# Kernel optimization log

Hardware: AMD Instinct MI355X
Metric: run time of the kernel (lower is better)

Reference implementation:

```python
import jax, jax.numpy as jnp
from jax import lax
import numpy as np

B, L, F = 4, 1024, 32
DM, NL, DS, DC, EX, NH = 256, 4, 16, 4, 2, 4
DI = EX * DM            # 512 inner channels
DTR = (DM + 15) // 16   # dt_rank = 16


def setup_inputs() -> dict:
    key = jax.random.key(0)
    ks = jax.random.split(key, 12)
    s = 0.02
    rn = lambda k, shape: jax.random.normal(k, shape, jnp.float32) * s
    return dict(
        x=jax.random.normal(ks[0], (B, L, F), jnp.float32),
        proj_w=rn(ks[1], (DM, F)), proj_b=jnp.zeros((DM,), jnp.float32),
        inproj_w=rn(ks[2], (NL, 2 * DI, DM)),
        conv_w=rn(ks[3], (NL, DI, DC)), conv_b=jnp.zeros((NL, DI), jnp.float32),
        xproj_w=rn(ks[4], (NL, DTR + 2 * DS, DI)),
        dtproj_w=rn(ks[5], (NL, DI, DTR)), dtproj_b=rn(ks[6], (NL, DI)),
        A_log=jnp.tile(jnp.log(jnp.arange(1, DS + 1, dtype=jnp.float32))[None, None, :], (NL, DI, 1)),
        Dp=jnp.ones((NL, DI), jnp.float32),
        outproj_w=rn(ks[7], (NL, DM, DI)),
        ln_g=jnp.ones((NL, DM), jnp.float32), ln_b=jnp.zeros((NL, DM), jnp.float32),
        head_w1=rn(ks[8], (DM, DM)), head_b1=jnp.zeros((DM,), jnp.float32),
        head_w2=rn(ks[9], (NH, DM)), head_b2=jnp.zeros((NH,), jnp.float32),
    )


def _layernorm(x, g, b, eps=1e-5):
    mu = x.mean(axis=-1, keepdims=True)
    var = ((x - mu) ** 2).mean(axis=-1, keepdims=True)
    return (x - mu) * lax.rsqrt(var + eps) * g + b


def _mamba(x, inw, cw, cb, xpw, dtw, dtb, A_log, Dp, outw):
    b, l, _ = x.shape
    xz = x @ inw.T                       # (b,l,2*DI)
    u, z = xz[..., :DI], xz[..., DI:]
    # causal depthwise conv1d, kernel DC
    up = jnp.pad(u, ((0, 0), (DC - 1, 0), (0, 0)))
    uc = sum(up[:, k:k + l, :] * cw[:, k] for k in range(DC)) + cb
    uc = jax.nn.silu(uc)
    dbc = uc @ xpw.T                     # (b,l,DTR+2*DS)
    dt, Bc, Cc = dbc[..., :DTR], dbc[..., DTR:DTR + DS], dbc[..., DTR + DS:]
    delta = jax.nn.softplus(dt @ dtw.T + dtb)   # (b,l,DI)
    A = -jnp.exp(A_log)                  # (DI,DS)

    def step(h, inp):
        d_t, B_t, C_t, u_t = inp         # (b,DI),(b,DS),(b,DS),(b,DI)
        h = jnp.exp(d_t[..., None] * A) * h + (d_t * u_t)[..., None] * B_t[:, None, :]
        return h, jnp.einsum('bdn,bn->bd', h, C_t)

    h0 = jnp.zeros((b, DI, DS), x.dtype)
    xs = tuple(jnp.swapaxes(a, 0, 1) for a in (delta, Bc, Cc, uc))
    _, ys = lax.scan(step, h0, xs)       # ys: (l,b,DI)
    y = jnp.swapaxes(ys, 0, 1) + uc * Dp
    return (y * jax.nn.silu(z)) @ outw.T


def reference(x, proj_w, proj_b, inproj_w, conv_w, conv_b, xproj_w, dtproj_w, dtproj_b,
              A_log, Dp, outproj_w, ln_g, ln_b, head_w1, head_b1, head_w2, head_b2):
    h = x @ proj_w.T + proj_b
    for i in range(NL):
        blk = _mamba(h, inproj_w[i], conv_w[i], conv_b[i], xproj_w[i],
                     dtproj_w[i], dtproj_b[i], A_log[i], Dp[i], outproj_w[i])
        h = h + _layernorm(blk, ln_g[i], ln_b[i])
    p = h.mean(axis=1)                   # (b,DM) pool over time
    hid = jax.nn.relu(p @ head_w1.T + head_b1)
    return hid @ head_w2.T + head_b2     # (b,NH)
```

## Files before the change

kernel.cpp:

```cpp
#include <hip/hip_runtime.h>
#include <hip/hip_fp16.h>
#include <math.h>

#define LTOT 1024
#define BB   4
#define F_IN 32
#define DM   256
#define DI   512
#define DS   16
#define DTRN 16
#define NXP  48
#define NLAY 4
#define NH   4
#define NC   16
#define CLEN 64
#define ROWS (BB*LTOT)

typedef _Float16 half8 __attribute__((ext_vector_type(8)));
typedef float f32x16 __attribute__((ext_vector_type(16)));
typedef unsigned short us8 __attribute__((ext_vector_type(8)));

__device__ __forceinline__ float siluf_(float x) { return x / (1.0f + expf(-x)); }
__device__ __forceinline__ float softplusf_(float x) {
    if (x > 20.f) return x;
    if (x < -20.f) return expf(x);
    return log1pf(expf(x));
}

__device__ __forceinline__ void split16(float x, unsigned short& hi, unsigned short& lo) {
    __half h = __float2half(x);
    hi = *(unsigned short*)&h;
    float r = x - __half2float(h);
    __half l = __float2half(r);
    lo = *(unsigned short*)&l;
}

__global__ __launch_bounds__(256) void k_init(const float* __restrict__ x,
                                              const float* __restrict__ pw,
                                              const float* __restrict__ pb,
                                              const float* __restrict__ inw,
                                              const float* __restrict__ outw,
                                              float* __restrict__ h,
                                              unsigned short* __restrict__ hh,
                                              unsigned short* __restrict__ hl,
                                              unsigned short* __restrict__ iwh,
                                              unsigned short* __restrict__ iwl,
                                              unsigned short* __restrict__ owh,
                                              unsigned short* __restrict__ owl) {
    __shared__ float wl[DM][33];
    __shared__ float xl[16][32];
    int bid = blockIdx.x, t = threadIdx.x;
    if (bid < 1536) {
        int q = bid * 256 + t;
        ushort4 h4, l4;
        if (q < 262144) {
            float4 v = ((const float4*)inw)[q];
            split16(v.x, h4.x, l4.x); split16(v.y, h4.y, l4.y);
            split16(v.z, h4.z, l4.z); split16(v.w, h4.w, l4.w);
            *(ushort4*)(iwh + (size_t)q * 4) = h4;
            *(ushort4*)(iwl + (size_t)q * 4) = l4;
        } else {
            int r = q - 262144;
            float4 v = ((const float4*)outw)[r];
            split16(v.x, h4.x, l4.x); split16(v.y, h4.y, l4.y);
            split16(v.z, h4.z, l4.z); split16(v.w, h4.w, l4.w);
            *(ushort4*)(owh + (size_t)r * 4) = h4;
            *(ushort4*)(owl + (size_t)r * 4) = l4;
        }
        return;
    }
    int r0 = (bid - 1536) * 16;
    for (int i = t; i < DM * 32 / 4; i += 256) {
        float4 v = ((const float4*)pw)[i];
        int c = i / 8, k = (i % 8) * 4;
        wl[c][k] = v.x; wl[c][k + 1] = v.y; wl[c][k + 2] = v.z; wl[c][k + 3] = v.w;
    }
    for (int i = t; i < 16 * 32 / 4; i += 256) {
        float4 v = ((const float4*)(x + (size_t)r0 * F_IN))[i];
        int r = i / 8, k = (i % 8) * 4;
        xl[r][k] = v.x; xl[r][k + 1] = v.y; xl[r][k + 2] = v.z; xl[r][k + 3] = v.w;
    }
    __syncthreads();
    int c = t;
    float bias = pb[c];
    float acc[16];
#pragma unroll
    for (int r = 0; r < 16; ++r) acc[r] = bias;
    for (int k = 0; k < 32; ++k) {
        float w = wl[c][k];
#pragma unroll
        for (int r = 0; r < 16; ++r) acc[r] = fmaf(xl[r][k], w, acc[r]);
    }
#pragma unroll
    for (int r = 0; r < 16; ++r) {
        size_t idx = (size_t)(r0 + r) * DM + c;
        h[idx] = acc[r];
        unsigned short vh, vl; split16(acc[r], vh, vl);
        hh[idx] = vh; hl[idx] = vl;
    }
}

__global__ __launch_bounds__(256) void k_gemm_xz(const unsigned short* __restrict__ Ahp,
                                                 const unsigned short* __restrict__ Alp,
                                                 const unsigned short* __restrict__ Bhp,
                                                 const unsigned short* __restrict__ Blp,
                                                 float* __restrict__ C) {
    __shared__ unsigned short Ah[64][40], Al[64][40], Bh[128][40], Bl[128][40];
    int t = threadIdx.x;
    int bx = blockIdx.x & 7;
    int by = blockIdx.x >> 3;
    int rowA = t >> 2, kA = (t & 3) * 8;
    int rowB = t >> 1, kB = (t & 1) * 16;
    const unsigned short* ApH = Ahp + (size_t)(by * 64 + rowA) * DM + kA;
    const unsigned short* ApL = Alp + (size_t)(by * 64 + rowA) * DM + kA;
    const unsigned short* BpH = Bhp + (size_t)(bx * 128 + rowB) * DM + kB;
    const unsigned short* BpL = Blp + (size_t)(bx * 128 + rowB) * DM + kB;
    us8 rah = *(const us8*)ApH, ral = *(const us8*)ApL;
    us8 rbh0 = *(const us8*)BpH, rbh1 = *(const us8*)(BpH + 8);
    us8 rbl0 = *(const us8*)BpL, rbl1 = *(const us8*)(BpL + 8);
    int lane = t & 63, wid = t >> 6;
    int fr = lane & 31, fg = lane >> 5;
    int wr = wid >> 1, wc = wid & 1;
    f32x16 acc[2] = {};
    for (int k0 = 0; k0 < DM; k0 += 32) {
        *(us8*)&Ah[rowA][kA] = rah;
        *(us8*)&Al[rowA][kA] = ral;
        *(us8*)&Bh[rowB][kB] = rbh0; *(us8*)&Bh[rowB][kB + 8] = rbh1;
        *(us8*)&Bl[rowB][kB] = rbl0; *(us8*)&Bl[rowB][kB + 8] = rbl1;
        __syncthreads();
        if (k0 + 32 < DM) {
            rah = *(const us8*)(ApH + k0 + 32); ral = *(const us8*)(ApL + k0 + 32);
            rbh0 = *(const us8*)(BpH + k0 + 32); rbh1 = *(const us8*)(BpH + k0 + 40);
            rbl0 = *(const us8*)(BpL + k0 + 32); rbl1 = *(const us8*)(BpL + k0 + 40);
        }
#pragma unroll
        for (int s = 0; s < 2; ++s) {
            int ko = s * 16 + fg * 8;
            half8 ah = *(const half8*)&Ah[wr * 32 + fr][ko];
            half8 al = *(const half8*)&Al[wr * 32 + fr][ko];
#pragma unroll
            for (int fc = 0; fc < 2; ++fc) {
                half8 bh = *(const half8*)&Bh[wc * 64 + fc * 32 + fr][ko];
                half8 bl = *(const half8*)&Bl[wc * 64 + fc * 32 + fr][ko];
                acc[fc] = __builtin_amdgcn_mfma_f32_32x32x16_f16(ah, bh, acc[fc], 0, 0, 0);
                acc[fc] = __builtin_amdgcn_mfma_f32_32x32x16_f16(ah, bl, acc[fc], 0, 0, 0);
                acc[fc] = __builtin_amdgcn_mfma_f32_32x32x16_f16(al, bh, acc[fc], 0, 0, 0);
            }
        }
        __syncthreads();
    }
    float* Cp = C + (size_t)(by * 64 + wr * 32) * 1024 + bx * 128 + wc * 64;
#pragma unroll
    for (int fc = 0; fc < 2; ++fc) {
#pragma unroll
        for (int reg = 0; reg < 16; ++reg) {
            int row = (reg & 3) + 8 * (reg >> 2) + 4 * fg;
            Cp[(size_t)row * 1024 + fc * 32 + fr] = acc[fc][reg];
        }
    }
}

__global__ __launch_bounds__(256) void k_dbcp(const float* __restrict__ xz,
                                              const float* __restrict__ cw,
                                              const float* __restrict__ cb,
                                              const float* __restrict__ xpw,
                                              float* __restrict__ uc,
                                              float* __restrict__ dbp) {
    __shared__ float us[32][132];
    __shared__ float wsd[48][132];
    int t = threadIdx.x;
    int kp = blockIdx.x & 3;
    int r0 = (blockIdx.x >> 2) * 32;
    int k0 = kp * 128;
    float4* us4 = (float4*)us;
    float4* ws4 = (float4*)wsd;
#pragma unroll
    for (int j = 0; j < 4; ++j) {
        int i = t + j * 256;
        int r = i >> 5, kq = i & 31;
        int rr = r0 + r, d = k0 + kq * 4;
        int tt = rr & (LTOT - 1);
        float4 acc = make_float4(cb[d], cb[d + 1], cb[d + 2], cb[d + 3]);
#pragma unroll
        for (int k = 0; k < 4; ++k) {
            int ts = tt - 3 + k;
            if (ts < 0) continue;
            float4 u = *(const float4*)(xz + (size_t)(rr - 3 + k) * 1024 + d);
            acc.x = fmaf(u.x, cw[(d + 0) * 4 + k], acc.x);
            acc.y = fmaf(u.y, cw[(d + 1) * 4 + k], acc.y);
            acc.z = fmaf(u.z, cw[(d + 2) * 4 + k], acc.z);
            acc.w = fmaf(u.w, cw[(d + 3) * 4 + k], acc.w);
        }
        acc.x = siluf_(acc.x); acc.y = siluf_(acc.y); acc.z = siluf_(acc.z); acc.w = siluf_(acc.w);
        us4[r * 33 + kq] = acc;
        *(float4*)(uc + (size_t)rr * DI + d) = acc;
    }
#pragma unroll
    for (int j = 0; j < 6; ++j) {
        int i = t + j * 256;
        int r = i >> 5, kq = i & 31;
        ws4[r * 33 + kq] = *(const float4*)(xpw + (size_t)r * DI + k0 + kq * 4);
    }
    __syncthreads();
    int tx = t & 15, ty = t >> 4;
    const float4* ua = us4 + (ty * 2) * 33;
    const float4* ub = ua + 33;
    const float4* w0p = ws4 + (tx * 3) * 33;
    const float4* w1p = w0p + 33;
    const float4* w2p = w0p + 66;
    float acc[2][3] = {};
#pragma unroll 4
    for (int kq = 0; kq < 32; ++kq) {
        float4 u0 = ua[kq], u1 = ub[kq];
        float4 w0 = w0p[kq], w1 = w1p[kq], w2 = w2p[kq];
        acc[0][0] = fmaf(u0.x, w0.x, acc[0][0]); acc[0][0] = fmaf(u0.y, w0.y, acc[0][0]);
        acc[0][0] = fmaf(u0.z, w0.z, acc[0][0]); acc[0][0] = fmaf(u0.w, w0.w, acc[0][0]);
        acc[0][1] = fmaf(u0.x, w1.x, acc[0][1]); acc[0][1] = fmaf(u0.y, w1.y, acc[0][1]);
        acc[0][1] = fmaf(u0.z, w1.z, acc[0][1]); acc[0][1] = fmaf(u0.w, w1.w, acc[0][1]);
        acc[0][2] = fmaf(u0.x, w2.x, acc[0][2]); acc[0][2] = fmaf(u0.y, w2.y, acc[0][2]);
        acc[0][2] = fmaf(u0.z, w2.z, acc[0][2]); acc[0][2] = fmaf(u0.w, w2.w, acc[0][2]);
        acc[1][0] = fmaf(u1.x, w0.x, acc[1][0]); acc[1][0] = fmaf(u1.y, w0.y, acc[1][0]);
        acc[1][0] = fmaf(u1.z, w0.z, acc[1][0]); acc[1][0] = fmaf(u1.w, w0.w, acc[1][0]);
        acc[1][1] = fmaf(u1.x, w1.x, acc[1][1]); acc[1][1] = fmaf(u1.y, w1.y, acc[1][1]);
        acc[1][1] = fmaf(u1.z, w1.z, acc[1][1]); acc[1][1] = fmaf(u1.w, w1.w, acc[1][1]);
        acc[1][2] = fmaf(u1.x, w2.x, acc[1][2]); acc[1][2] = fmaf(u1.y, w2.y, acc[1][2]);
        acc[1][2] = fmaf(u1.z, w2.z, acc[1][2]); acc[1][2] = fmaf(u1.w, w2.w, acc[1][2]);
    }
    float* outp = dbp + (size_t)(r0 + ty * 2) * 192 + kp * 48 + tx * 3;
    outp[0] = acc[0][0]; outp[1] = acc[0][1]; outp[2] = acc[0][2];
    outp[192] = acc[1][0]; outp[193] = acc[1][1]; outp[194] = acc[1][2];
}

__global__ __launch_bounds__(256) void k_scanA(const float* __restrict__ dbp,
                                               const float* __restrict__ uc,
                                               const float* __restrict__ dtw,
                                               const float* __restrict__ dtb,
                                               const float* __restrict__ A_log,
                                               float* __restrict__ P,
                                               float* __restrict__ hL) {
    __shared__ float2 du2[CLEN][16];
    __shared__ float  Bl[CLEN][16];
    __shared__ float  dbl[CLEN][17];
    __shared__ float  wdl[16][17];
    __shared__ float  wbias[16];
    int bid = blockIdx.x;
    int c = bid & 15, dblk = (bid >> 4) & 31, b = bid >> 9;
    int d0 = dblk * 16, t0 = c * CLEN;
    int t = threadIdx.x;
    int row = t >> 2, q4 = (t & 3) * 4;
    size_t rbase = (size_t)(b * LTOT + t0 + row);
    float4 uv = *(const float4*)(uc + rbase * DI + d0 + q4);
    {
        const float* pp = dbp + rbase * 192;
        float4 a0 = *(const float4*)(pp + q4);
        float4 a1 = *(const float4*)(pp + 48 + q4);
        float4 a2 = *(const float4*)(pp + 96 + q4);
        float4 a3 = *(const float4*)(pp + 144 + q4);
        dbl[row][q4 + 0] = ((a0.x + a1.x) + a2.x) + a3.x;
        dbl[row][q4 + 1] = ((a0.y + a1.y) + a2.y) + a3.y;
        dbl[row][q4 + 2] = ((a0.z + a1.z) + a2.z) + a3.z;
        dbl[row][q4 + 3] = ((a0.w + a1.w) + a2.w) + a3.w;
        float4 b0 = *(const float4*)(pp + 16 + q4);
        float4 b1 = *(const float4*)(pp + 64 + q4);
        float4 b2 = *(const float4*)(pp + 112 + q4);
        float4 b3 = *(const float4*)(pp + 160 + q4);
        Bl[row][q4 + 0] = ((b0.x + b1.x) + b2.x) + b3.x;
        Bl[row][q4 + 1] = ((b0.y + b1.y) + b2.y) + b3.y;
        Bl[row][q4 + 2] = ((b0.z + b1.z) + b2.z) + b3.z;
        Bl[row][q4 + 3] = ((b0.w + b1.w) + b2.w) + b3.w;
    }
    if (t < 64) {
        int dd = t >> 2, sg = (t & 3) * 4;
        const float* wp = dtw + (size_t)(d0 + dd) * 16 + sg;
        wdl[dd][sg + 0] = wp[0]; wdl[dd][sg + 1] = wp[1];
        wdl[dd][sg + 2] = wp[2]; wdl[dd][sg + 3] = wp[3];
    }
    if (t < 16) wbias[t] = dtb[d0 + t];
    __syncthreads();
    {
        float s0 = wbias[q4 + 0], s1 = wbias[q4 + 1], s2 = wbias[q4 + 2], s3 = wbias[q4 + 3];
#pragma unroll
        for (int k = 0; k < 16; ++k) {
            float dv = dbl[row][k];
            s0 = fmaf(dv, wdl[q4 + 0][k], s0);
            s1 = fmaf(dv, wdl[q4 + 1][k], s1);
            s2 = fmaf(dv, wdl[q4 + 2][k], s2);
            s3 = fmaf(dv, wdl[q4 + 3][k], s3);
        }
        du2[row][q4 + 0] = make_float2(softplusf_(s0), uv.x);
        du2[row][q4 + 1] = make_float2(softplusf_(s1), uv.y);
        du2[row][q4 + 2] = make_float2(softplusf_(s2), uv.z);
        du2[row][q4 + 3] = make_float2(softplusf_(s3), uv.w);
    }
    __syncthreads();
    int n = t & 15, dn = t >> 4;
    float Ac = -expf(A_log[(size_t)(d0 + dn) * DS + n]);
    float h = 0.f, Pp = 1.f;
#pragma unroll 8
    for (int k = 0; k < CLEN; ++k) {
        float2 du = du2[k][dn];
        float Bv = Bl[k][n];
        float a = expf(du.x * Ac);
        Pp *= a;
        h = fmaf(a, h, du.x * du.y * Bv);
    }
    size_t idx = ((size_t)(b * NC + c)) * (DI * DS) + (size_t)d0 * DS + t;
    P[idx] = Pp;
    hL[idx] = h;
}

__global__ __launch_bounds__(256) void k_scanC(const float* __restrict__ dbp,
                                               const float* __restrict__ uc,
                                               const float* __restrict__ dtw,
                                               const float* __restrict__ dtb,
                                               const float* __restrict__ A_log,
                                               const float* __restrict__ P,
                                               const float* __restrict__ hL,
                                               const float* __restrict__ Dp,
                                               const float* __restrict__ xz,
                                               unsigned short* __restrict__ yh,
                                               unsigned short* __restrict__ yl) {
    __shared__ float2 du2[CLEN][16];
    __shared__ float2 bc2[CLEN][16];
    __shared__ float  ytmp[16][16][20];
    float* scr = &ytmp[0][0][0];
    float (*dbl)[17] = (float(*)[17])scr;
    float (*wdl)[17] = (float(*)[17])(scr + 1088);
    float* wbias = scr + 1088 + 272;
    int bid = blockIdx.x;
    int c = bid & 15, dblk = (bid >> 4) & 31, b = bid >> 9;
    int d0 = dblk * 16, t0 = c * CLEN;
    int t = threadIdx.x;
    int row = t >> 2, q4 = (t & 3) * 4;
    size_t rbase = (size_t)(b * LTOT + t0 + row);
    float4 uv = *(const float4*)(uc + rbase * DI + d0 + q4);
    {
        const float* pp = dbp + rbase * 192;
        float4 a0 = *(const float4*)(pp + q4);
        float4 a1 = *(const float4*)(pp + 48 + q4);
        float4 a2 = *(const float4*)(pp + 96 + q4);
        float4 a3 = *(const float4*)(pp + 144 + q4);
        dbl[row][q4 + 0] = ((a0.x + a1.x) + a2.x) + a3.x;
        dbl[row][q4 + 1] = ((a0.y + a1.y) + a2.y) + a3.y;
        dbl[row][q4 + 2] = ((a0.z + a1.z) + a2.z) + a3.z;
        dbl[row][q4 + 3] = ((a0.w + a1.w) + a2.w) + a3.w;
        float4 b0 = *(const float4*)(pp + 16 + q4);
        float4 b1 = *(const float4*)(pp + 64 + q4);
        float4 b2 = *(const float4*)(pp + 112 + q4);
        float4 b3 = *(const float4*)(pp + 160 + q4);
        float4 c0 = *(const float4*)(pp + 32 + q4);
        float4 c1 = *(const float4*)(pp + 80 + q4);
        float4 c2 = *(const float4*)(pp + 128 + q4);
        float4 c3 = *(const float4*)(pp + 176 + q4);
        float B0 = ((b0.x + b1.x) + b2.x) + b3.x, C0 = ((c0.x + c1.x) + c2.x) + c3.x;
        float B1 = ((b0.y + b1.y) + b2.y) + b3.y, C1 = ((c0.y + c1.y) + c2.y) + c3.y;
        float B2 = ((b0.z + b1.z) + b2.z) + b3.z, C2 = ((c0.z + c1.z) + c2.z) + c3.z;
        float B3 = ((b0.w + b1.w) + b2.w) + b3.w, C3 = ((c0.w + c1.w) + c2.w) + c3.w;
        bc2[row][q4 + 0] = make_float2(B0, C0);
        bc2[row][q4 + 1] = make_float2(B1, C1);
        bc2[row][q4 + 2] = make_float2(B2, C2);
        bc2[row][q4 + 3] = make_float2(B3, C3);
    }
    if (t < 64) {
        int dd = t >> 2, sg = (t & 3) * 4;
        const float* wp = dtw + (size_t)(d0 + dd) * 16 + sg;
        wdl[dd][sg + 0] = wp[0]; wdl[dd][sg + 1] = wp[1];
        wdl[dd][sg + 2] = wp[2]; wdl[dd][sg + 3] = wp[3];
    }
    if (t < 16) wbias[t] = dtb[d0 + t];
    __syncthreads();
    {
        float s0 = wbias[q4 + 0], s1 = wbias[q4 + 1], s2 = wbias[q4 + 2], s3 = wbias[q4 + 3];
#pragma unroll
        for (int k = 0; k < 16; ++k) {
            float dv = dbl[row][k];
            s0 = fmaf(dv, wdl[q4 + 0][k], s0);
            s1 = fmaf(dv, wdl[q4 + 1][k], s1);
            s2 = fmaf(dv, wdl[q4 + 2][k], s2);
            s3 = fmaf(dv, wdl[q4 + 3][k], s3);
        }
        du2[row][q4 + 0] = make_float2(softplusf_(s0), uv.x);
        du2[row][q4 + 1] = make_float2(softplusf_(s1), uv.y);
        du2[row][q4 + 2] = make_float2(softplusf_(s2), uv.z);
        du2[row][q4 + 3] = make_float2(softplusf_(s3), uv.w);
    }
    __syncthreads();
    int n = t & 15, dn = t >> 4;
    float Ac = -expf(A_log[(size_t)(d0 + dn) * DS + n]);
    float Hin = 0.f;
    for (int cc = 0; cc < c; ++cc) {
        size_t idx = ((size_t)(b * NC + cc)) * (DI * DS) + (size_t)d0 * DS + t;
        Hin = fmaf(P[idx], Hin, hL[idx]);
    }
    float h = Hin;
    int rdn = t & 15, rk = t >> 4;
    float DpV = Dp[d0 + rdn];
    for (int s = 0; s < CLEN / 16; ++s) {
#pragma unroll
        for (int kk = 0; kk < 16; ++kk) {
            int k = s * 16 + kk;
            float2 du = du2[k][dn];
            float2 bc = bc2[k][n];
            float a = expf(du.x * Ac);
            h = fmaf(a, h, du.x * du.y * bc.x);
            ytmp[kk][dn][n] = h * bc.y;
        }
        __syncthreads();
        {
            const float* rowp = &ytmp[rk][rdn][0];
            float4 v0 = *(const float4*)(rowp + 0);
            float4 v1 = *(const float4*)(rowp + 4);
            float4 v2 = *(const float4*)(rowp + 8);
            float4 v3 = *(const float4*)(rowp + 12);
            float y = ((v0.x + v0.y) + (v0.z + v0.w)) + ((v1.x + v1.y) + (v1.z + v1.w))
                    + ((v2.x + v2.y) + (v2.z + v2.w)) + ((v3.x + v3.y) + (v3.z + v3.w));
            float uu = du2[s * 16 + rk][rdn].y;
            size_t rb2 = (size_t)(b * LTOT + t0 + s * 16 + rk);
            float z = xz[rb2 * 1024 + 512 + d0 + rdn];
            float val = fmaf(uu, DpV, y) * siluf_(z);
            unsigned short vh, vl; split16(val, vh, vl);
            size_t yi = rb2 * DI + d0 + rdn;
            yh[yi] = vh; yl[yi] = vl;
        }
        __syncthreads();
    }
}

__global__ __launch_bounds__(256) void k_gemm_out(const unsigned short* __restrict__ Ahp,
                                                  const unsigned short* __restrict__ Alp,
                                                  const unsigned short* __restrict__ Bhp,
                                                  const unsigned short* __restrict__ Blp,
                                                  float* __restrict__ p01,
                                                  float* __restrict__ p23) {
    __shared__ unsigned short Ah[64][40], Al[64][40], Bh[128][40], Bl[128][40];
    int t = threadIdx.x;
    int bx = blockIdx.x & 1;
    int by = (blockIdx.x >> 1) & 63;
    int kp = blockIdx.x >> 7;
    int rowA = t >> 2, kA = (t & 3) * 8;
    int rowB = t >> 1, kB = (t & 1) * 16;
    const unsigned short* ApH = Ahp + (size_t)(by * 64 + rowA) * DI + kp * 128 + kA;
    const unsigned short* ApL = Alp + (size_t)(by * 64 + rowA) * DI + kp * 128 + kA;
    const unsigned short* BpH = Bhp + (size_t)(bx * 128 + rowB) * DI + kp * 128 + kB;
    const unsigned short* BpL = Blp + (size_t)(bx * 128 + rowB) * DI + kp * 128 + kB;
    us8 rah = *(const us8*)ApH, ral = *(const us8*)ApL;
    us8 rbh0 = *(const us8*)BpH, rbh1 = *(const us8*)(BpH + 8);
    us8 rbl0 = *(const us8*)BpL, rbl1 = *(const us8*)(BpL + 8);
    int lane = t & 63, wid = t >> 6;
    int fr = lane & 31, fg = lane >> 5;
    int wr = wid >> 1, wc = wid & 1;
    f32x16 acc[2] = {};
    for (int k0 = 0; k0 < 128; k0 += 32) {
        *(us8*)&Ah[rowA][kA] = rah;
        *(us8*)&Al[rowA][kA] = ral;
        *(us8*)&Bh[rowB][kB] = rbh0; *(us8*)&Bh[rowB][kB + 8] = rbh1;
        *(us8*)&Bl[rowB][kB] = rbl0; *(us8*)&Bl[rowB][kB + 8] = rbl1;
        __syncthreads();
        if (k0 + 32 < 128) {
            rah = *(const us8*)(ApH + k0 + 32); ral = *(const us8*)(ApL + k0 + 32);
            rbh0 = *(const us8*)(BpH + k0 + 32); rbh1 = *(const us8*)(BpH + k0 + 40);
            rbl0 = *(const us8*)(BpL + k0 + 32); rbl1 = *(const us8*)(BpL + k0 + 40);
        }
#pragma unroll
        for (int s = 0; s < 2; ++s) {
            int ko = s * 16 + fg * 8;
            half8 ah = *(const half8*)&Ah[wr * 32 + fr][ko];
            half8 al = *(const half8*)&Al[wr * 32 + fr][ko];
#pragma unroll
            for (int fc = 0; fc < 2; ++fc) {
                half8 bh = *(const half8*)&Bh[wc * 64 + fc * 32 + fr][ko];
                half8 bl = *(const half8*)&Bl[wc * 64 + fc * 32 + fr][ko];
                acc[fc] = __builtin_amdgcn_mfma_f32_32x32x16_f16(ah, bh, acc[fc], 0, 0, 0);
                acc[fc] = __builtin_amdgcn_mfma_f32_32x32x16_f16(ah, bl, acc[fc], 0, 0, 0);
                acc[fc] = __builtin_amdgcn_mfma_f32_32x32x16_f16(al, bh, acc[fc], 0, 0, 0);
            }
        }
        __syncthreads();
    }
    float* pbase = (kp < 2 ? p01 : p23) + (size_t)(kp & 1) * (ROWS * DM);
    float* Cp = pbase + (size_t)(by * 64 + wr * 32) * DM + bx * 128 + wc * 64;
#pragma unroll
    for (int fc = 0; fc < 2; ++fc) {
#pragma unroll
        for (int reg = 0; reg < 16; ++reg) {
            int row = (reg & 3) + 8 * (reg >> 2) + 4 * fg;
            Cp[(size_t)row * DM + fc * 32 + fr] = acc[fc][reg];
        }
    }
}

__global__ __launch_bounds__(256) void k_ln_res(const float* __restrict__ p01,
                                                const float* __restrict__ p23,
                                                const float* __restrict__ g,
                                                const float* __restrict__ bb,
                                                float* __restrict__ h,
                                                unsigned short* __restrict__ hh,
                                                unsigned short* __restrict__ hl) {
    __shared__ float scratch[4];
    int r = blockIdx.x, t = threadIdx.x;
    size_t idx = (size_t)r * DM + t;
    float v = p01[idx] + p01[idx + (size_t)ROWS * DM] + p23[idx] + p23[idx + (size_t)ROWS * DM];
    float s = v;
#pragma unroll
    for (int m = 32; m >= 1; m >>= 1) s += __shfl_xor(s, m, 64);
    if ((t & 63) == 0) scratch[t >> 6] = s;
    __syncthreads();
    float mu = (scratch[0] + scratch[1] + scratch[2] + scratch[3]) * (1.f / DM);
    __syncthreads();
    float d = v - mu;
    float s2 = d * d;
#pragma unroll
    for (int m = 32; m >= 1; m >>= 1) s2 += __shfl_xor(s2, m, 64);
    if ((t & 63) == 0) scratch[t >> 6] = s2;
    __syncthreads();
    float var = (scratch[0] + scratch[1] + scratch[2] + scratch[3]) * (1.f / DM);
    float rstd = 1.f / sqrtf(var + 1e-5f);
    float nv = h[idx] + d * rstd * g[t] + bb[t];
    h[idx] = nv;
    unsigned short vh, vl; split16(nv, vh, vl);
    hh[idx] = vh; hl[idx] = vl;
}

__global__ __launch_bounds__(256) void k_meanp(const float* __restrict__ h,
                                               float* __restrict__ part) {
    int bid = blockIdx.x;
    int b = bid >> 3, g = bid & 7;
    int t = threadIdx.x;
    float s = 0.f;
    for (int k = 0; k < 128; ++k)
        s += h[(size_t)(b * LTOT + g * 128 + k) * DM + t];
    part[(size_t)bid * DM + t] = s;
}

__global__ __launch_bounds__(256) void k_head(const float* __restrict__ part,
                                              const float* __restrict__ w1,
                                              const float* __restrict__ b1,
                                              const float* __restrict__ w2,
                                              const float* __restrict__ b2,
                                              float* __restrict__ out) {
    __shared__ float pl[DM], hl[DM];
    int b = blockIdx.x, t = threadIdx.x;
    float s = 0.f;
    for (int g = 0; g < 8; ++g) s += part[(size_t)(b * 8 + g) * DM + t];
    pl[t] = s * (1.f / LTOT);
    __syncthreads();
    float a = b1[t];
    for (int k = 0; k < DM; ++k) a = fmaf(pl[k], w1[(size_t)t * DM + k], a);
    hl[t] = fmaxf(a, 0.f);
    __syncthreads();
    if (t < NH) {
        float o = b2[t];
        for (int k = 0; k < DM; ++k) o = fmaf(hl[k], w2[(size_t)t * DM + k], o);
        out[b * NH + t] = o;
    }
}

extern "C" void kernel_launch(void* const* d_in, const int* in_sizes, int n_in,
                              void* d_out, int out_size, void* d_ws, size_t ws_size,
                              hipStream_t stream) {
    const float* x        = (const float*)d_in[0];
    const float* proj_w   = (const float*)d_in[1];
    const float* proj_b   = (const float*)d_in[2];
    const float* inproj_w = (const float*)d_in[3];
    const float* conv_w   = (const float*)d_in[4];
    const float* conv_b   = (const float*)d_in[5];
    const float* xproj_w  = (const float*)d_in[6];
    const float* dtproj_w = (const float*)d_in[7];
    const float* dtproj_b = (const float*)d_in[8];
    const float* A_log    = (const float*)d_in[9];
    const float* Dp       = (const float*)d_in[10];
    const float* outproj_w= (const float*)d_in[11];
    const float* ln_g     = (const float*)d_in[12];
    const float* ln_b     = (const float*)d_in[13];
    const float* head_w1  = (const float*)d_in[14];
    const float* head_b1  = (const float*)d_in[15];
    const float* head_w2  = (const float*)d_in[16];
    const float* head_b2  = (const float*)d_in[17];

    float* ws    = (float*)d_ws;
    float* h     = ws;
    float* xz    = h + 1048576;
    float* uc    = xz + 4194304;
    float* dbp   = uc + 2097152;
    float* Pbuf  = dbp + 786432;
    float* hLbuf = Pbuf + 524288;
    float* p01   = hLbuf + 524288;
    float* p23   = p01 + 2097152;
    float* part  = p23 + 2097152;
    unsigned short* h_hi  = (unsigned short*)(part + 8192);
    unsigned short* h_lo  = h_hi + 1048576;
    unsigned short* y_hi  = h_lo + 1048576;
    unsigned short* y_lo  = y_hi + 2097152;
    unsigned short* iw_hi = y_lo + 2097152;
    unsigned short* iw_lo = iw_hi + 1048576;
    unsigned short* ow_hi = iw_lo + 1048576;
    unsigned short* ow_lo = ow_hi + 524288;

    k_init<<<1792, 256, 0, stream>>>(x, proj_w, proj_b, inproj_w, outproj_w,
                                     h, h_hi, h_lo, iw_hi, iw_lo, ow_hi, ow_lo);

    for (int i = 0; i < NLAY; ++i) {
        const float* cwi  = conv_w + (size_t)i * DI * 4;
        const float* cbi  = conv_b + (size_t)i * DI;
        const float* xpw  = xproj_w + (size_t)i * NXP * DI;
        const float* dtw  = dtproj_w + (size_t)i * DI * DTRN;
        const float* dtb  = dtproj_b + (size_t)i * DI;
        const float* Ali  = A_log + (size_t)i * DI * DS;
        const float* Dpi  = Dp + (size_t)i * DI;
        const float* gi   = ln_g + (size_t)i * DM;
        const float* bi   = ln_b + (size_t)i * DM;

        k_gemm_xz<<<512, 256, 0, stream>>>(h_hi, h_lo,
                                           iw_hi + (size_t)i * 262144, iw_lo + (size_t)i * 262144, xz);
        k_dbcp<<<512, 256, 0, stream>>>(xz, cwi, cbi, xpw, uc, dbp);
        k_scanA<<<BB * 32 * NC, 256, 0, stream>>>(dbp, uc, dtw, dtb, Ali, Pbuf, hLbuf);
        k_scanC<<<BB * 32 * NC, 256, 0, stream>>>(dbp, uc, dtw, dtb, Ali, Pbuf, hLbuf, Dpi, xz, y_hi, y_lo);
        k_gemm_out<<<512, 256, 0, stream>>>(y_hi, y_lo,
                                            ow_hi + (size_t)i * 131072, ow_lo + (size_t)i * 131072,
                                            p01, p23);
        k_ln_res<<<ROWS, 256, 0, stream>>>(p01, p23, gi, bi, h, h_hi, h_lo);
    }

    k_meanp<<<32, 256, 0, stream>>>(h, part);
    k_head<<<BB, 256, 0, stream>>>(part, head_w1, head_b1, head_w2, head_b2, (float*)d_out);
}
```

Measured before the change: 482.7 us.

## Store GEMM operands in MFMA fragment order and load directly from global

Producers of the split-fp16 operands (weights, hidden state, scan output) now write them in a pre-swizzled MFMA fragment layout. The in_proj and out_proj GEMMs then drop shared-memory staging and barriers, and each lane loads its half8 fragment straight from global memory with register double-buffering. This aims to remove LDS traffic and syncs. The cost is no cross-wave reuse through LDS, so each wave re-reads the A/B fragments from global/L2, and producer stores become scattered 2-byte writes.

```diff
diff --git a/kernel.cpp b/kernel.cpp
--- a/kernel.cpp
+++ b/kernel.cpp
@@ -18,7 +18,6 @@
 
 typedef _Float16 half8 __attribute__((ext_vector_type(8)));
 typedef float f32x16 __attribute__((ext_vector_type(16)));
-typedef unsigned short us8 __attribute__((ext_vector_type(8)));
 
 __device__ __forceinline__ float siluf_(float x) { return x / (1.0f + expf(-x)); }
 __device__ __forceinline__ float softplusf_(float x) {
@@ -33,6 +32,11 @@
     float r = x - __half2float(h);
     __half l = __float2half(r);
     lo = *(unsigned short*)&l;
+}
+
+__device__ __forceinline__ size_t fragAddr(int r, int k, int Kd) {
+    return ((size_t)((r >> 5) * (Kd >> 4) + (k >> 4)) << 9)
+         + (size_t)(((((k >> 3) & 1) << 5) + (r & 31)) * 8 + (k & 7));
 }
 
 __global__ __launch_bounds__(256) void k_init(const float* __restrict__ x,
@@ -57,15 +61,21 @@
             float4 v = ((const float4*)inw)[q];
             split16(v.x, h4.x, l4.x); split16(v.y, h4.y, l4.y);
             split16(v.z, h4.z, l4.z); split16(v.w, h4.w, l4.w);
-            *(ushort4*)(iwh + (size_t)q * 4) = h4;
-            *(ushort4*)(iwl + (size_t)q * 4) = l4;
+            int row = q >> 6, k0 = (q & 63) * 4;
+            int lay = row >> 10, rIn = row & 1023;
+            size_t fa = (size_t)lay * 262144 + fragAddr(rIn, k0, 256);
+            *(ushort4*)(iwh + fa) = h4;
+            *(ushort4*)(iwl + fa) = l4;
         } else {
-            int r = q - 262144;
-            float4 v = ((const float4*)outw)[r];
+            int rq = q - 262144;
+            float4 v = ((const float4*)outw)[rq];
             split16(v.x, h4.x, l4.x); split16(v.y, h4.y, l4.y);
             split16(v.z, h4.z, l4.z); split16(v.w, h4.w, l4.w);
-            *(ushort4*)(owh + (size_t)r * 4) = h4;
-            *(ushort4*)(owl + (size_t)r * 4) = l4;
+            int row = rq >> 7, k0 = (rq & 127) * 4;
+            int lay = row >> 8, rIn = row & 255;
+            size_t fa = (size_t)lay * 131072 + fragAddr(rIn, k0, 512);
+            *(ushort4*)(owh + fa) = h4;
+            *(ushort4*)(owl + fa) = l4;
         }
         return;
     }
@@ -93,10 +103,11 @@
     }
 #pragma unroll
     for (int r = 0; r < 16; ++r) {
-        size_t idx = (size_t)(r0 + r) * DM + c;
-        h[idx] = acc[r];
+        int rr = r0 + r;
+        h[(size_t)rr * DM + c] = acc[r];
         unsigned short vh, vl; split16(acc[r], vh, vl);
-        hh[idx] = vh; hl[idx] = vl;
+        size_t fa = fragAddr(rr, c, 256);
+        hh[fa] = vh; hl[fa] = vl;
     }
 }
 
@@ -105,49 +116,39 @@
                                                  const unsigned short* __restrict__ Bhp,
                                                  const unsigned short* __restrict__ Blp,
                                                  float* __restrict__ C) {
-    __shared__ unsigned short Ah[64][40], Al[64][40], Bh[128][40], Bl[128][40];
     int t = threadIdx.x;
     int bx = blockIdx.x & 7;
     int by = blockIdx.x >> 3;
-    int rowA = t >> 2, kA = (t & 3) * 8;
-    int rowB = t >> 1, kB = (t & 1) * 16;
-    const unsigned short* ApH = Ahp + (size_t)(by * 64 + rowA) * DM + kA;
-    const unsigned short* ApL = Alp + (size_t)(by * 64 + rowA) * DM + kA;
-    const unsigned short* BpH = Bhp + (size_t)(bx * 128 + rowB) * DM + kB;
-    const unsigned short* BpL = Blp + (size_t)(bx * 128 + rowB) * DM + kB;
-    us8 rah = *(const us8*)ApH, ral = *(const us8*)ApL;
-    us8 rbh0 = *(const us8*)BpH, rbh1 = *(const us8*)(BpH + 8);
-    us8 rbl0 = *(const us8*)BpL, rbl1 = *(const us8*)(BpL + 8);
     int lane = t & 63, wid = t >> 6;
     int fr = lane & 31, fg = lane >> 5;
     int wr = wid >> 1, wc = wid & 1;
+    int rt = by * 2 + wr;
+    int ct0 = bx * 4 + wc * 2;
+    const half8* pAh = (const half8*)Ahp + (size_t)rt * 1024 + lane;
+    const half8* pAl = (const half8*)Alp + (size_t)rt * 1024 + lane;
+    const half8* pB0h = (const half8*)Bhp + (size_t)ct0 * 1024 + lane;
+    const half8* pB0l = (const half8*)Blp + (size_t)ct0 * 1024 + lane;
+    const half8* pB1h = pB0h + 1024;
+    const half8* pB1l = pB0l + 1024;
     f32x16 acc[2] = {};
-    for (int k0 = 0; k0 < DM; k0 += 32) {
-        *(us8*)&Ah[rowA][kA] = rah;
-        *(us8*)&Al[rowA][kA] = ral;
-        *(us8*)&Bh[rowB][kB] = rbh0; *(us8*)&Bh[rowB][kB + 8] = rbh1;
-        *(us8*)&Bl[rowB][kB] = rbl0; *(us8*)&Bl[rowB][kB + 8] = rbl1;
-        __syncthreads();
-        if (k0 + 32 < DM) {
-            rah = *(const us8*)(ApH + k0 + 32); ral = *(const us8*)(ApL + k0 + 32);
-            rbh0 = *(const us8*)(BpH + k0 + 32); rbh1 = *(const us8*)(BpH + k0 + 40);
-            rbl0 = *(const us8*)(BpL + k0 + 32); rbl1 = *(const us8*)(BpL + k0 + 40);
-        }
-#pragma unroll
-        for (int s = 0; s < 2; ++s) {
-            int ko = s * 16 + fg * 8;
-            half8 ah = *(const half8*)&Ah[wr * 32 + fr][ko];
-            half8 al = *(const half8*)&Al[wr * 32 + fr][ko];
-#pragma unroll
-            for (int fc = 0; fc < 2; ++fc) {
-                half8 bh = *(const half8*)&Bh[wc * 64 + fc * 32 + fr][ko];
-                half8 bl = *(const half8*)&Bl[wc * 64 + fc * 32 + fr][ko];
-                acc[fc] = __builtin_amdgcn_mfma_f32_32x32x16_f16(ah, bh, acc[fc], 0, 0, 0);
-                acc[fc] = __builtin_amdgcn_mfma_f32_32x32x16_f16(ah, bl, acc[fc], 0, 0, 0);
-                acc[fc] = __builtin_amdgcn_mfma_f32_32x32x16_f16(al, bh, acc[fc], 0, 0, 0);
-            }
-        }
-        __syncthreads();
+    half8 ah = pAh[0], al = pAl[0];
+    half8 b0h = pB0h[0], b0l = pB0l[0], b1h = pB1h[0], b1l = pB1l[0];
+#pragma unroll
+    for (int kt = 0; kt < 16; ++kt) {
+        half8 nah, nal, nb0h, nb0l, nb1h, nb1l;
+        if (kt < 15) {
+            int o = (kt + 1) * 64;
+            nah = pAh[o]; nal = pAl[o];
+            nb0h = pB0h[o]; nb0l = pB0l[o];
+            nb1h = pB1h[o]; nb1l = pB1l[o];
+        }
+        acc[0] = __builtin_amdgcn_mfma_f32_32x32x16_f16(ah, b0h, acc[0], 0, 0, 0);
+        acc[0] = __builtin_amdgcn_mfma_f32_32x32x16_f16(ah, b0l, acc[0], 0, 0, 0);
+        acc[0] = __builtin_amdgcn_mfma_f32_32x32x16_f16(al, b0h, acc[0], 0, 0, 0);
+        acc[1] = __builtin_amdgcn_mfma_f32_32x32x16_f16(ah, b1h, acc[1], 0, 0, 0);
+        acc[1] = __builtin_amdgcn_mfma_f32_32x32x16_f16(ah, b1l, acc[1], 0, 0, 0);
+        acc[1] = __builtin_amdgcn_mfma_f32_32x32x16_f16(al, b1h, acc[1], 0, 0, 0);
+        if (kt < 15) { ah = nah; al = nal; b0h = nb0h; b0l = nb0l; b1h = nb1h; b1l = nb1l; }
     }
     float* Cp = C + (size_t)(by * 64 + wr * 32) * 1024 + bx * 128 + wc * 64;
 #pragma unroll
@@ -419,8 +420,8 @@
             float z = xz[rb2 * 1024 + 512 + d0 + rdn];
             float val = fmaf(uu, DpV, y) * siluf_(z);
             unsigned short vh, vl; split16(val, vh, vl);
-            size_t yi = rb2 * DI + d0 + rdn;
-            yh[yi] = vh; yl[yi] = vl;
+            size_t fa = fragAddr((int)rb2, d0 + rdn, 512);
+            yh[fa] = vh; yl[fa] = vl;
         }
         __syncthreads();
     }
@@ -432,50 +433,40 @@
                                                   const unsigned short* __restrict__ Blp,
                                                   float* __restrict__ p01,
                                                   float* __restrict__ p23) {
-    __shared__ unsigned short Ah[64][40], Al[64][40], Bh[128][40], Bl[128][40];
     int t = threadIdx.x;
     int bx = blockIdx.x & 1;
     int by = (blockIdx.x >> 1) & 63;
     int kp = blockIdx.x >> 7;
-    int rowA = t >> 2, kA = (t & 3) * 8;
-    int rowB = t >> 1, kB = (t & 1) * 16;
-    const unsigned short* ApH = Ahp + (size_t)(by * 64 + rowA) * DI + kp * 128 + kA;
-    const unsigned short* ApL = Alp + (size_t)(by * 64 + rowA) * DI + kp * 128 + kA;
-    const unsigned short* BpH = Bhp + (size_t)(bx * 128 + rowB) * DI + kp * 128 + kB;
-    const unsigned short* BpL = Blp + (size_t)(bx * 128 + rowB) * DI + kp * 128 + kB;
-    us8 rah = *(const us8*)ApH, ral = *(const us8*)ApL;
-    us8 rbh0 = *(const us8*)BpH, rbh1 = *(const us8*)(BpH + 8);
-    us8 rbl0 = *(const us8*)BpL, rbl1 = *(const us8*)(BpL + 8);
     int lane = t & 63, wid = t >> 6;
     int fr = lane & 31, fg = lane >> 5;
     int wr = wid >> 1, wc = wid & 1;
+    int rt = by * 2 + wr;
+    int ct0 = bx * 4 + wc * 2;
+    const half8* pAh = (const half8*)Ahp + (size_t)rt * 2048 + (size_t)kp * 512 + lane;
+    const half8* pAl = (const half8*)Alp + (size_t)rt * 2048 + (size_t)kp * 512 + lane;
+    const half8* pB0h = (const half8*)Bhp + (size_t)ct0 * 2048 + (size_t)kp * 512 + lane;
+    const half8* pB0l = (const half8*)Blp + (size_t)ct0 * 2048 + (size_t)kp * 512 + lane;
+    const half8* pB1h = pB0h + 2048;
+    const half8* pB1l = pB0l + 2048;
     f32x16 acc[2] = {};
-    for (int k0 = 0; k0 < 128; k0 += 32) {
-        *(us8*)&Ah[rowA][kA] = rah;
-        *(us8*)&Al[rowA][kA] = ral;
-        *(us8*)&Bh[rowB][kB] = rbh0; *(us8*)&Bh[rowB][kB + 8] = rbh1;
-        *(us8*)&Bl[rowB][kB] = rbl0; *(us8*)&Bl[rowB][kB + 8] = rbl1;
-        __syncthreads();
-        if (k0 + 32 < 128) {
-            rah = *(const us8*)(ApH + k0 + 32); ral = *(const us8*)(ApL + k0 + 32);
-            rbh0 = *(const us8*)(BpH + k0 + 32); rbh1 = *(const us8*)(BpH + k0 + 40);
-            rbl0 = *(const us8*)(BpL + k0 + 32); rbl1 = *(const us8*)(BpL + k0 + 40);
-        }
-#pragma unroll
-        for (int s = 0; s < 2; ++s) {
-            int ko = s * 16 + fg * 8;
-            half8 ah = *(const half8*)&Ah[wr * 32 + fr][ko];
-            half8 al = *(const half8*)&Al[wr * 32 + fr][ko];
-#pragma unroll
-            for (int fc = 0; fc < 2; ++fc) {
-                half8 bh = *(const half8*)&Bh[wc * 64 + fc * 32 + fr][ko];
-                half8 bl = *(const half8*)&Bl[wc * 64 + fc * 32 + fr][ko];
-                acc[fc] = __builtin_amdgcn_mfma_f32_32x32x16_f16(ah, bh, acc[fc], 0, 0, 0);
-                acc[fc] = __builtin_amdgcn_mfma_f32_32x32x16_f16(ah, bl, acc[fc], 0, 0, 0);
-                acc[fc] = __builtin_amdgcn_mfma_f32_32x32x16_f16(al, bh, acc[fc], 0, 0, 0);
-            }
-        }
-        __syncthreads();
+    half8 ah = pAh[0], al = pAl[0];
+    half8 b0h = pB0h[0], b0l = pB0l[0], b1h = pB1h[0], b1l = pB1l[0];
+#pragma unroll
+    for (int kt = 0; kt < 8; ++kt) {
+        half8 nah, nal, nb0h, nb0l, nb1h, nb1l;
+        if (kt < 7) {
+            int o = (kt + 1) * 64;
+            nah = pAh[o]; nal = pAl[o];
+            nb0h = pB0h[o]; nb0l = pB0l[o];
+            nb1h = pB1h[o]; nb1l = pB1l[o];
+        }
+        acc[0] = __builtin_amdgcn_mfma_f32_32x32x16_f16(ah, b0h, acc[0], 0, 0, 0);
+        acc[0] = __builtin_amdgcn_mfma_f32_32x32x16_f16(ah, b0l, acc[0], 0, 0, 0);
+        acc[0] = __builtin_amdgcn_mfma_f32_32x32x16_f16(al, b0h, acc[0], 0, 0, 0);
+        acc[1] = __builtin_amdgcn_mfma_f32_32x32x16_f16(ah, b1h, acc[1], 0, 0, 0);
+        acc[1] = __builtin_amdgcn_mfma_f32_32x32x16_f16(ah, b1l, acc[1], 0, 0, 0);
+        acc[1] = __builtin_amdgcn_mfma_f32_32x32x16_f16(al, b1h, acc[1], 0, 0, 0);
+        if (kt < 7) { ah = nah; al = nal; b0h = nb0h; b0l = nb0l; b1h = nb1h; b1l = nb1l; }
     }
     float* pbase = (kp < 2 ? p01 : p23) + (size_t)(kp & 1) * (ROWS * DM);
     float* Cp = pbase + (size_t)(by * 64 + wr * 32) * DM + bx * 128 + wc * 64;
@@ -518,7 +509,8 @@
     float nv = h[idx] + d * rstd * g[t] + bb[t];
     h[idx] = nv;
     unsigned short vh, vl; split16(nv, vh, vl);
-    hh[idx] = vh; hl[idx] = vl;
+    size_t fa = fragAddr(r, t, 256);
+    hh[fa] = vh; hl[fa] = vl;
 }
 
 __global__ __launch_bounds__(256) void k_meanp(const float* __restrict__ h,
```

New measurement: 494.8 us. 2.5% more time.
